# Kernel optimization log

Measured on AMD Instinct MI355X. Metric: run time of the kernel, lower is better.

Reference implementation:

```python
import jax, jax.numpy as jnp
import numpy as np

T, B, IN, H, L = 512, 64, 512, 512, 2


def setup_inputs() -> dict:
    key = jax.random.key(0)
    k1, k2, k3, k4 = jax.random.split(key, 4)
    s = 1.0 / np.sqrt(H)
    return {
        "x": jax.random.normal(k1, (T, B, IN), dtype=jnp.float32),
        "Wx": jax.random.normal(k2, (L, 4 * H, IN), dtype=jnp.float32) * s,
        "Wh": jax.random.normal(k3, (L, 4 * H, H), dtype=jnp.float32) * s,
        "bh": jax.random.normal(k4, (L, 4 * H), dtype=jnp.float32) * s,
    }


def reference(x, Wx, Wh, bh):
    n_layers = Wh.shape[0]
    hidden = Wh.shape[2]
    batch = x.shape[1]
    h0 = jnp.zeros((n_layers, batch, hidden), dtype=x.dtype)
    c0 = jnp.zeros((n_layers, batch, hidden), dtype=x.dtype)

    def step(carry, x_t):
        h, c = carry  # [L,B,H] each
        inp = x_t
        hs, cs = [], []
        for l in range(n_layers):
            # ifgo: [B, 4H]
            ifgo = inp @ Wx[l].T + h[l] @ Wh[l].T + bh[l]
            i = jax.nn.sigmoid(ifgo[:, :hidden])
            f = jax.nn.sigmoid(ifgo[:, hidden:2 * hidden])
            g = jnp.tanh(ifgo[:, 2 * hidden:3 * hidden])
            o = jax.nn.sigmoid(ifgo[:, 3 * hidden:])
            c_next = f * c[l] + i * g
            h_next = o * jnp.tanh(c_next)
            hs.append(h_next)
            cs.append(c_next)
            inp = h_next
        return (jnp.stack(hs), jnp.stack(cs)), hs[-1]

    (h, c), out = jax.lax.scan(step, (h0, c0), x)
    return out, h, c
```

## Files before the change

### kernel.cpp

```cpp
#include <hip/hip_runtime.h>


typedef unsigned short u16;
typedef unsigned int u32;
typedef unsigned long long u64;
typedef __attribute__((ext_vector_type(8))) short bf16x8;
typedef __attribute__((ext_vector_type(4))) float floatx4;
typedef __attribute__((ext_vector_type(16))) float floatx16;

#define T_ 512
#define B_ 64
#define H_ 512
#define BH (B_ * H_)

__device__ __forceinline__ u16 f2bf(float f) {
  u32 u = __float_as_uint(f);
  u32 r = (u + 0x7fffu + ((u >> 16) & 1u)) >> 16;
  return (u16)r;
}

__device__ __forceinline__ float sigm(float x) { return 1.f / (1.f + __expf(-x)); }

__device__ __forceinline__ float tanh_(float x) {
  float ax = fabsf(x);
  float e = __expf(-2.f * ax);
  float t = (1.f - e) / (1.f + e);
  return copysignf(t, x);
}

__global__ void conv_w_kernel(const float* __restrict__ Wx, const float* __restrict__ Wh,
                              u16* __restrict__ Wcat) {
  int i = blockIdx.x * 256 + threadIdx.x;
  int base = i * 4;
  int k = base & 1023;
  int row = base >> 10;
  const float* src = (k < 512) ? (Wx + row * 512 + k) : (Wh + row * 512 + (k - 512));
  float4 v = *(const float4*)src;
  uint2 p;
  p.x = (u32)f2bf(v.x) | ((u32)f2bf(v.y) << 16);
  p.y = (u32)f2bf(v.z) | ((u32)f2bf(v.w) << 16);
  *(uint2*)(Wcat + base) = p;
}

__global__ void conv_x_kernel(const float* __restrict__ x, u16* __restrict__ xb) {
  int p = blockIdx.x * 256 + threadIdx.x;
  int L = p & 63;
  int i = (p >> 6) & 31;
  int bt = (p >> 11) & 1;
  int t = p >> 12;
  int r = bt * 32 + (L & 31);
  int k0 = i * 16 + (L >> 5) * 8;
  const float* s = x + ((size_t)(t * 64 + r) * 512 + k0);
  float4 v0 = *(const float4*)s;
  float4 v1 = *(const float4*)(s + 4);
  uint4 q;
  q.x = (u32)f2bf(v0.x) | ((u32)f2bf(v0.y) << 16);
  q.y = (u32)f2bf(v0.z) | ((u32)f2bf(v0.w) << 16);
  q.z = (u32)f2bf(v1.x) | ((u32)f2bf(v1.y) << 16);
  q.w = (u32)f2bf(v1.z) | ((u32)f2bf(v1.w) << 16);
  *(uint4*)(xb + (size_t)p * 8) = q;
}

__global__ void init_flags(u32* flags) {
  if (threadIdx.x < 256) flags[threadIdx.x] = 0;
}

__device__ __forceinline__ u32 aload32(const u32* p) {
  return __hip_atomic_load(p, __ATOMIC_RELAXED, __HIP_MEMORY_SCOPE_AGENT);
}
__device__ __forceinline__ u64 aload64(const u64* p) {
  return __hip_atomic_load(p, __ATOMIC_RELAXED, __HIP_MEMORY_SCOPE_AGENT);
}
__device__ __forceinline__ void astore32(u32* p, u32 v) {
  __hip_atomic_store(p, v, __ATOMIC_RELAXED, __HIP_MEMORY_SCOPE_AGENT);
}
__device__ __forceinline__ void astore64(u64* p, u64 v) {
  __hip_atomic_store(p, v, __ATOMIC_RELAXED, __HIP_MEMORY_SCOPE_AGENT);
}

__device__ __forceinline__ void wave_wait(const u32* f, u32 target, int lane) {
  while (!__all((int)(aload32(f + lane) >= target))) __builtin_amdgcn_s_sleep(1);
}

__device__ __forceinline__ void consume_dense(const u64* __restrict__ hb, const bf16x8* w,
                                              floatx16& acc, int lane) {
  u64 q0[32], q1[32];
#pragma unroll
  for (int i = 0; i < 32; ++i) {
    q0[i] = aload64(hb + i * 128 + lane * 2);
    q1[i] = aload64(hb + i * 128 + lane * 2 + 1);
  }
#pragma unroll
  for (int i = 0; i < 32; ++i) {
    union {
      u64 qq[2];
      bf16x8 v;
    } u;
    u.qq[0] = q0[i];
    u.qq[1] = q1[i];
    acc = __builtin_amdgcn_mfma_f32_32x32x16_bf16(w[i], u.v, acc, 0, 0, 0);
  }
}

__global__ __launch_bounds__(256, 1) void lstm_persist(
    const u16* __restrict__ Wcat, const float* __restrict__ bh,
    const u16* __restrict__ xb, u16* __restrict__ h0s, u16* __restrict__ h1s,
    u32* flags, float* __restrict__ out) {
  const int unit = blockIdx.x & 1;
  const int cg = blockIdx.x >> 1;
  const int colbase = cg * 8;
  const int tid = threadIdx.x;
  const int wave = tid >> 6;
  const int bt = wave & 1;
  const int kh = wave >> 1;
  const int lane = tid & 63;
  const int l31 = lane & 31;
  const int lh = lane >> 5;

  __shared__ float ldsp[2 * 2 * 4 * 256];

  bf16x8 w[32];
  {
    const int rp = l31;
    const u16* wbase = Wcat + ((size_t)unit * 2048 + (rp >> 3) * 512 + colbase + (rp & 7)) * 1024 +
                       kh * 512 + lh * 8;
#pragma unroll
    for (int i = 0; i < 32; ++i) w[i] = *(const bf16x8*)(wbase + i * 16);
  }

  float bias[4][4];
#pragma unroll
  for (int g = 0; g < 4; ++g)
#pragma unroll
    for (int q = 0; q < 4; ++q)
      bias[g][q] = bh[unit * 2048 + g * 512 + colbase + 4 * lh + q];
  float creg[4] = {0.f, 0.f, 0.f, 0.f};

  u32* f0 = flags;
  u32* f1 = flags + 128;
  u32* myflag = (unit ? f1 : f0) + bt * 64 + cg;

  const size_t out_h_base = (size_t)T_ * BH;
  const size_t out_c_base = out_h_base + 2 * (size_t)BH;
  const int orow = bt * 32 + l31;
  const int ocol = colbase + 4 * lh;

  const size_t pub_idx =
      ((size_t)bt * 2048 + (cg >> 1) * 64 + (cg & 1) * 32 + l31) * 2 + lh;

  for (int t = 0; t < T_; ++t) {
    floatx16 acc = {0.f, 0.f, 0.f, 0.f, 0.f, 0.f, 0.f, 0.f,
                    0.f, 0.f, 0.f, 0.f, 0.f, 0.f, 0.f, 0.f};
    const int buf = t & 1;
    float* lp = ldsp + (buf * 2 + bt) * 1024 + lane * 4;

    if (kh == 0) {
      if (unit == 0) {
        const bf16x8* xp = (const bf16x8*)xb + (size_t)t * 4096 + bt * 2048 + lane;
#pragma unroll
        for (int i = 0; i < 32; ++i)
          acc = __builtin_amdgcn_mfma_f32_32x32x16_bf16(w[i], xp[i * 64], acc, 0, 0, 0);
      } else {
        wave_wait(f0 + bt * 64, (u32)(t + 1), lane);
        consume_dense((const u64*)h0s + (size_t)(t & 3) * 8192 + (size_t)bt * 4096, w, acc, lane);
      }
#pragma unroll
      for (int rg = 0; rg < 4; ++rg)
        *(floatx4*)(lp + rg * 256) =
            floatx4{acc[rg * 4 + 0], acc[rg * 4 + 1], acc[rg * 4 + 2], acc[rg * 4 + 3]};
      __syncthreads();
    } else {
      if (t > 0) {
        if (unit == 0) {
          wave_wait(f0 + bt * 64, (u32)t, lane);
          consume_dense((const u64*)h0s + (size_t)((t - 1) & 3) * 8192 + (size_t)bt * 4096, w,
                        acc, lane);
        } else {
          wave_wait(f1 + bt * 64, (u32)t, lane);
          consume_dense((const u64*)h1s + (size_t)((t - 1) & 3) * 8192 + (size_t)bt * 4096, w,
                        acc, lane);
        }
      }
      __syncthreads();
#pragma unroll
      for (int rg = 0; rg < 4; ++rg) {
        floatx4 p = *(const floatx4*)(lp + rg * 256);
        acc[rg * 4 + 0] += p.x;
        acc[rg * 4 + 1] += p.y;
        acc[rg * 4 + 2] += p.z;
        acc[rg * 4 + 3] += p.w;
      }
      float hn[4], cn[4];
#pragma unroll
      for (int q = 0; q < 4; ++q) {
        float pi = acc[q] + bias[0][q];
        float pf = acc[4 + q] + bias[1][q];
        float pg = acc[8 + q] + bias[2][q];
        float po = acc[12 + q] + bias[3][q];
        float ig = sigm(pi);
        float fg = sigm(pf);
        float gg = tanh_(pg);
        float og = sigm(po);
        cn[q] = fg * creg[q] + ig * gg;
        hn[q] = og * tanh_(cn[q]);
        creg[q] = cn[q];
      }

      if (unit == 0 && t >= 4) wave_wait(f1 + bt * 64, (u32)(t - 3), lane);

      u64 pack = (u64)f2bf(hn[0]) | ((u64)f2bf(hn[1]) << 16) | ((u64)f2bf(hn[2]) << 32) |
                 ((u64)f2bf(hn[3]) << 48);
      u64* slot = (u64*)((unit ? h1s : h0s) + (size_t)(t & 3) * BH);
      astore64(slot + pub_idx, pack);
      asm volatile("s_waitcnt vmcnt(0)" ::: "memory");
      if (lane == 0) astore32(myflag, (u32)(t + 1));

      if (unit == 1)
        *(float4*)(out + (size_t)t * BH + (size_t)orow * 512 + ocol) =
            make_float4(hn[0], hn[1], hn[2], hn[3]);
      if (t == T_ - 1) {
        *(float4*)(out + out_h_base + (size_t)unit * BH + (size_t)orow * 512 + ocol) =
            make_float4(hn[0], hn[1], hn[2], hn[3]);
        *(float4*)(out + out_c_base + (size_t)unit * BH + (size_t)orow * 512 + ocol) =
            make_float4(cn[0], cn[1], cn[2], cn[3]);
      }
    }
  }
}

extern "C" void kernel_launch(void* const* d_in, const int* in_sizes, int n_in,
                              void* d_out, int out_size, void* d_ws, size_t ws_size,
                              hipStream_t stream) {
  const float* x = (const float*)d_in[0];
  const float* Wx = (const float*)d_in[1];
  const float* Wh = (const float*)d_in[2];
  const float* bh = (const float*)d_in[3];
  float* out = (float*)d_out;
  char* ws = (char*)d_ws;

  u16* Wcat = (u16*)ws;
  u16* xb = (u16*)(ws + 8388608);
  u16* h0s = (u16*)(ws + 8388608 + 33554432);
  u16* h1s = (u16*)(ws + 8388608 + 33554432 + 262144);
  u32* flags = (u32*)(ws + 8388608 + 33554432 + 2 * 262144);

  conv_w_kernel<<<4096, 256, 0, stream>>>(Wx, Wh, Wcat);
  conv_x_kernel<<<8192, 256, 0, stream>>>(x, xb);
  init_flags<<<1, 256, 0, stream>>>(flags);
  lstm_persist<<<128, 256, 0, stream>>>(Wcat, bh, xb, h0s, h1s, flags, out);
}
```

Measured before the change: 3.933 ms.

## Fan out per-consumer progress flags and spin without sleeping

Replaces the single shared flag array with private per-block flag copies. Each producing wave now writes its progress counter into every consumer block's slot, using all 64 lanes for two stores each. Consumers poll only their own flags, and the s_sleep in the spin loop is removed. The aim is to cut contention and polling latency on the shared flag cache lines in the per-timestep cross-block handshake. In exchange, each wave issues many more atomic stores per step, and the tighter spin adds memory traffic.

```diff
diff --git a/kernel.cpp b/kernel.cpp
--- a/kernel.cpp
+++ b/kernel.cpp
@@ -61,8 +61,8 @@
   *(uint4*)(xb + (size_t)p * 8) = q;
 }
 
-__global__ void init_flags(u32* flags) {
-  if (threadIdx.x < 256) flags[threadIdx.x] = 0;
+__global__ void init_flags(u32* pf) {
+  pf[blockIdx.x * 256 + threadIdx.x] = 0;
 }
 
 __device__ __forceinline__ u32 aload32(const u32* p) {
@@ -79,7 +79,8 @@
 }
 
 __device__ __forceinline__ void wave_wait(const u32* f, u32 target, int lane) {
-  while (!__all((int)(aload32(f + lane) >= target))) __builtin_amdgcn_s_sleep(1);
+  while (!__all((int)(aload32(f + lane) >= target))) {
+  }
 }
 
 __device__ __forceinline__ void consume_dense(const u64* __restrict__ hb, const bf16x8* w,
@@ -105,9 +106,10 @@
 __global__ __launch_bounds__(256, 1) void lstm_persist(
     const u16* __restrict__ Wcat, const float* __restrict__ bh,
     const u16* __restrict__ xb, u16* __restrict__ h0s, u16* __restrict__ h1s,
-    u32* flags, float* __restrict__ out) {
-  const int unit = blockIdx.x & 1;
-  const int cg = blockIdx.x >> 1;
+    u32* pf0, u32* pf1, float* __restrict__ out) {
+  const int blk = blockIdx.x;
+  const int unit = blk & 1;
+  const int cg = blk >> 1;
   const int colbase = cg * 8;
   const int tid = threadIdx.x;
   const int wave = tid >> 6;
@@ -136,9 +138,11 @@
       bias[g][q] = bh[unit * 2048 + g * 512 + colbase + 4 * lh + q];
   float creg[4] = {0.f, 0.f, 0.f, 0.f};
 
-  u32* f0 = flags;
-  u32* f1 = flags + 128;
-  u32* myflag = (unit ? f1 : f0) + bt * 64 + cg;
+  const u32* my_pf0 = pf0 + (blk * 2 + bt) * 64;
+  const u32* my_pf1 = pf1 + (blk * 2 + bt) * 64;
+  u32* fan_base = (unit ? pf1 : pf0);
+  u32* fan_a = fan_base + ((size_t)lane * 2 + bt) * 64 + cg;
+  u32* fan_b = fan_base + (((size_t)lane + 64) * 2 + bt) * 64 + cg;
 
   const size_t out_h_base = (size_t)T_ * BH;
   const size_t out_c_base = out_h_base + 2 * (size_t)BH;
@@ -161,7 +165,7 @@
         for (int i = 0; i < 32; ++i)
           acc = __builtin_amdgcn_mfma_f32_32x32x16_bf16(w[i], xp[i * 64], acc, 0, 0, 0);
       } else {
-        wave_wait(f0 + bt * 64, (u32)(t + 1), lane);
+        wave_wait(my_pf0, (u32)(t + 1), lane);
         consume_dense((const u64*)h0s + (size_t)(t & 3) * 8192 + (size_t)bt * 4096, w, acc, lane);
       }
 #pragma unroll
@@ -172,11 +176,11 @@
     } else {
       if (t > 0) {
         if (unit == 0) {
-          wave_wait(f0 + bt * 64, (u32)t, lane);
+          wave_wait(my_pf0, (u32)t, lane);
           consume_dense((const u64*)h0s + (size_t)((t - 1) & 3) * 8192 + (size_t)bt * 4096, w,
                         acc, lane);
         } else {
-          wave_wait(f1 + bt * 64, (u32)t, lane);
+          wave_wait(my_pf1, (u32)t, lane);
           consume_dense((const u64*)h1s + (size_t)((t - 1) & 3) * 8192 + (size_t)bt * 4096, w,
                         acc, lane);
         }
@@ -206,14 +210,15 @@
         creg[q] = cn[q];
       }
 
-      if (unit == 0 && t >= 4) wave_wait(f1 + bt * 64, (u32)(t - 3), lane);
+      if (unit == 0 && t >= 4) wave_wait(my_pf1, (u32)(t - 3), lane);
 
       u64 pack = (u64)f2bf(hn[0]) | ((u64)f2bf(hn[1]) << 16) | ((u64)f2bf(hn[2]) << 32) |
                  ((u64)f2bf(hn[3]) << 48);
       u64* slot = (u64*)((unit ? h1s : h0s) + (size_t)(t & 3) * BH);
       astore64(slot + pub_idx, pack);
       asm volatile("s_waitcnt vmcnt(0)" ::: "memory");
-      if (lane == 0) astore32(myflag, (u32)(t + 1));
+      astore32(fan_a, (u32)(t + 1));
+      astore32(fan_b, (u32)(t + 1));
 
       if (unit == 1)
         *(float4*)(out + (size_t)t * BH + (size_t)orow * 512 + ocol) =
@@ -242,10 +247,11 @@
   u16* xb = (u16*)(ws + 8388608);
   u16* h0s = (u16*)(ws + 8388608 + 33554432);
   u16* h1s = (u16*)(ws + 8388608 + 33554432 + 262144);
-  u32* flags = (u32*)(ws + 8388608 + 33554432 + 2 * 262144);
+  u32* pf0 = (u32*)(ws + 8388608 + 33554432 + 2 * 262144);
+  u32* pf1 = (u32*)(ws + 8388608 + 33554432 + 2 * 262144 + 131072);
 
   conv_w_kernel<<<4096, 256, 0, stream>>>(Wx, Wh, Wcat);
   conv_x_kernel<<<8192, 256, 0, stream>>>(x, xb);
-  init_flags<<<1, 256, 0, stream>>>(flags);
-  lstm_persist<<<128, 256, 0, stream>>>(Wcat, bh, xb, h0s, h1s, flags, out);
-}
+  init_flags<<<256, 256, 0, stream>>>(pf0);
+  lstm_persist<<<128, 256, 0, stream>>>(Wcat, bh, xb, h0s, h1s, pf0, pf1, out);
+}
```

Result: faster. 3.354 ms (-14.7%).
